# Kernel tuning notes

Measured on AMD Instinct MI355X. Metric: run time of the kernel, lower is better.

The kernel has to match this reference:

```python
import jax, jax.numpy as jnp
import numpy as np

N, E, C_IN, HID, G, L = 100000, 1600000, 64, 32, 128, 3
NEG_SLOPE = 0.01  # F.leaky_relu default


def setup_inputs() -> dict:
    key = jax.random.key(0)
    ks = jax.random.split(key, 10)
    x = jax.random.normal(ks[0], (N, C_IN), dtype=jnp.float32)
    src = jax.random.randint(ks[1], (E,), 0, N, dtype=jnp.int32)
    dst = jax.random.randint(ks[2], (E,), 0, N, dtype=jnp.int32)
    batch = jnp.sort(jax.random.randint(ks[3], (N,), 0, G, dtype=jnp.int32))
    def glorot(k, fan_in, fan_out):
        lim = np.sqrt(6.0 / (fan_in + fan_out)).astype(np.float32)
        return jax.random.uniform(k, (fan_in, fan_out), jnp.float32, -lim, lim)
    W0 = glorot(ks[4], C_IN, HID); b0 = jnp.zeros((HID,), jnp.float32)
    W1 = glorot(ks[5], HID, HID);  b1 = jnp.zeros((HID,), jnp.float32)
    W2 = glorot(ks[6], HID, HID);  b2 = jnp.zeros((HID,), jnp.float32)
    return {"x": x, "W0": W0, "b0": b0, "W1": W1, "b1": b1,
            "W2": W2, "b2": b2, "src": src, "dst": dst, "batch": batch}


def _gcn_conv(x, W, b, src, dst, dinv):
    # PyG GCNConv: h = x W; aggregate with sym-norm (A + I)
    h = x @ W                                   # [N, H]
    coef = (dinv[src] * dinv[dst])[:, None]     # [E, 1]
    msg = h[src] * coef                         # gather + scale
    agg = jax.ops.segment_sum(msg, dst, num_segments=N)
    agg = agg + h * (dinv * dinv)[:, None]      # self-loop term
    return agg + b


def _mean_pool(x, batch, counts):
    s = jax.ops.segment_sum(x, batch, num_segments=G)
    return s / counts[:, None]


def reference(x, W0, b0, W1, b1, W2, b2, src, dst, batch):
    # degree with self loops (edge weight 1), as PyG gcn_norm does
    deg = jax.ops.segment_sum(jnp.ones((E,), x.dtype), dst, num_segments=N) + 1.0
    dinv = jax.lax.rsqrt(deg)
    counts = jnp.maximum(
        jax.ops.segment_sum(jnp.ones((N,), x.dtype), batch, num_segments=G), 1.0)
    params = [(W0, b0), (W1, b1), (W2, b2)]
    feats = []
    h = x
    for W, b in params:
        h = _gcn_conv(h, W, b, src, dst, dinv)
        h = jax.nn.leaky_relu(h, NEG_SLOPE)
        feats.append(_mean_pool(h, batch, counts))
    merge = jnp.mean(jnp.stack(feats, axis=0), axis=0)  # [G, HID]
    return merge
```

## Files before the change

### kernel.cpp

```cpp
#include <hip/hip_runtime.h>
#include <hip/hip_bf16.h>

#define NN 100000
#define NE 1600000
#define CIN 64
#define HIDN 32
#define NG 128
#define SLOPE 0.01f

__global__ __launch_bounds__(256) void k_cnt(const int* __restrict__ batch,
                                             float* __restrict__ cinv) {
  __shared__ int sb[NG + 1];
  int g = threadIdx.x;
  if (g <= NG) {
    int lo = 0, hi = NN;
    while (lo < hi) {
      int mid = (lo + hi) >> 1;
      if (batch[mid] < g) lo = mid + 1; else hi = mid;
    }
    sb[g] = lo;
  }
  __syncthreads();
  if (g < NG) {
    int c = sb[g + 1] - sb[g];
    cinv[g] = 1.0f / (3.0f * fmaxf((float)c, 1.0f));
  }
}


__global__ __launch_bounds__(256) void k_rank(const int* __restrict__ dst,
                                              int* __restrict__ deg,
                                              int* __restrict__ rank) {
  int i = blockIdx.x * 256 + threadIdx.x;
  if (i * 4 >= NE) return;
  int4 d = ((const int4*)dst)[i];
  int4 r;
  r.x = atomicAdd(&deg[d.x], 1);
  r.y = atomicAdd(&deg[d.y], 1);
  r.z = atomicAdd(&deg[d.z], 1);
  r.w = atomicAdd(&deg[d.w], 1);
  ((int4*)rank)[i] = r;
}

__global__ __launch_bounds__(256) void k_norm(const int* __restrict__ deg,
                                              float* __restrict__ dinv) {
  int i = blockIdx.x * 256 + threadIdx.x;
  if (i < NN) dinv[i] = rsqrtf((float)deg[i] + 1.0f);
}


__global__ __launch_bounds__(256) void k_scan1(const int* __restrict__ deg,
                                               int* __restrict__ bsum) {
  __shared__ int s[256];
  int t = threadIdx.x;
  int base = blockIdx.x * 1024 + t * 4;
  int sum = 0;
#pragma unroll
  for (int j = 0; j < 4; ++j) {
    int idx = base + j;
    if (idx < NN) sum += deg[idx];
  }
  s[t] = sum;
  __syncthreads();
  for (int o = 128; o > 0; o >>= 1) {
    if (t < o) s[t] += s[t + o];
    __syncthreads();
  }
  if (t == 0) bsum[blockIdx.x] = s[0];
}

__global__ __launch_bounds__(128) void k_scan2(int* __restrict__ bsum,
                                               int* __restrict__ rowp, int nblk) {
  __shared__ int s[128];
  int t = threadIdx.x;
  if (t < nblk) s[t] = bsum[t];
  __syncthreads();
  if (t == 0) {
    int run = 0;
    for (int i = 0; i < nblk; ++i) {
      int v = s[i];
      s[i] = run;
      run += v;
    }
    rowp[NN] = run;
  }
  __syncthreads();
  if (t < nblk) bsum[t] = s[t];
}

__global__ __launch_bounds__(256) void k_scan3(const int* __restrict__ deg,
                                               const int* __restrict__ bsum,
                                               int* __restrict__ rowp) {
  __shared__ int s[256];
  int t = threadIdx.x;
  int base = blockIdx.x * 1024 + t * 4;
  int d0 = 0, d1 = 0, d2 = 0, d3 = 0;
  if (base < NN) d0 = deg[base];
  if (base + 1 < NN) d1 = deg[base + 1];
  if (base + 2 < NN) d2 = deg[base + 2];
  if (base + 3 < NN) d3 = deg[base + 3];
  int ts = d0 + d1 + d2 + d3;
  s[t] = ts;
  __syncthreads();
  for (int o = 1; o < 256; o <<= 1) {
    int v = (t >= o) ? s[t - o] : 0;
    __syncthreads();
    s[t] += v;
    __syncthreads();
  }
  int run = bsum[blockIdx.x] + s[t] - ts;
  if (base < NN) { rowp[base] = run; run += d0; }
  if (base + 1 < NN) { rowp[base + 1] = run; run += d1; }
  if (base + 2 < NN) { rowp[base + 2] = run; run += d2; }
  if (base + 3 < NN) { rowp[base + 3] = run; run += d3; }
}

__global__ __launch_bounds__(256) void k_scatter(const int* __restrict__ src,
                                                 const int* __restrict__ dst,
                                                 const int* __restrict__ rank,
                                                 const int* __restrict__ rowp,
                                                 int* __restrict__ col) {
  int i = blockIdx.x * 256 + threadIdx.x;
  if (i * 4 >= NE) return;
  int4 d = ((const int4*)dst)[i];
  int4 r = ((const int4*)rank)[i];
  int4 s = ((const int4*)src)[i];
  col[rowp[d.x] + r.x] = s.x;
  col[rowp[d.y] + r.y] = s.y;
  col[rowp[d.z] + r.z] = s.z;
  col[rowp[d.w] + r.w] = s.w;
}


template <int K>
__global__ __launch_bounds__(256) void k_mm(const float* __restrict__ in,
                                            const float* __restrict__ W,
                                            const float* __restrict__ dinv,
                                            __hip_bfloat16* __restrict__ out) {
  __shared__ float sW[K * HIDN];
  int t = threadIdx.x;
  for (int i = t; i < K * HIDN; i += 256) sW[i] = W[i];
  __syncthreads();
  int gid = blockIdx.x * 256 + t;
  int node = gid >> 5;
  int f = gid & 31;
  if (node >= NN) return;
  const float* xr = in + node * K;
  float acc = 0.f;
#pragma unroll
  for (int k = 0; k < K; ++k) acc += xr[k] * sW[k * HIDN + f];
  out[node * HIDN + f] = __float2bfloat16(acc * dinv[node]);
}


template <int WRITE_H>
__global__ __launch_bounds__(256) void k_agg(const __hip_bfloat16* __restrict__ hs,
                                             const int* __restrict__ rowp,
                                             const int* __restrict__ col,
                                             const float* __restrict__ dinv,
                                             const int* __restrict__ batch,
                                             const float* __restrict__ cinv,
                                             const float* __restrict__ bias,
                                             float* __restrict__ hout,
                                             float* __restrict__ pool) {
  const int t = threadIdx.x;
  const int f = t & 31;
  const int sub = t >> 5;
  const float bf = bias[f];
  float pacc = 0.f;
  int gcur = -1;
  const int base = blockIdx.x * 32;
#pragma unroll
  for (int it = 0; it < 4; ++it) {
    const int i = base + it * 8 + sub;
    if (i < NN) {
      float acc = __bfloat162float(hs[i * HIDN + f]);
      const int rs = rowp[i];
      const int re = rowp[i + 1];
      int e = rs;
      for (; e + 4 <= re; e += 4) {
        const int c0 = col[e], c1 = col[e + 1], c2 = col[e + 2], c3 = col[e + 3];
        const float v0 = __bfloat162float(hs[c0 * HIDN + f]);
        const float v1 = __bfloat162float(hs[c1 * HIDN + f]);
        const float v2 = __bfloat162float(hs[c2 * HIDN + f]);
        const float v3 = __bfloat162float(hs[c3 * HIDN + f]);
        acc += (v0 + v1) + (v2 + v3);
      }
      for (; e < re; ++e) acc += __bfloat162float(hs[col[e] * HIDN + f]);
      float v = acc * dinv[i] + bf;
      v = v > 0.f ? v : SLOPE * v;
      if (WRITE_H) hout[i * HIDN + f] = v;
      const int g = batch[i];
      if (g != gcur) {
        if (gcur >= 0) unsafeAtomicAdd(&pool[gcur * HIDN + f], pacc * cinv[gcur]);
        gcur = g;
        pacc = 0.f;
      }
      pacc += v;
    }
  }
  if (gcur >= 0) unsafeAtomicAdd(&pool[gcur * HIDN + f], pacc * cinv[gcur]);
}


extern "C" void kernel_launch(void* const* d_in, const int* in_sizes, int n_in,
                              void* d_out, int out_size, void* d_ws, size_t ws_size,
                              hipStream_t stream) {
  const float* x = (const float*)d_in[0];
  const float* W0 = (const float*)d_in[1];
  const float* b0 = (const float*)d_in[2];
  const float* W1 = (const float*)d_in[3];
  const float* b1 = (const float*)d_in[4];
  const float* W2 = (const float*)d_in[5];
  const float* b2 = (const float*)d_in[6];
  const int* src = (const int*)d_in[7];
  const int* dst = (const int*)d_in[8];
  const int* batch = (const int*)d_in[9];
  float* out = (float*)d_out;

  char* ws = (char*)d_ws;
  auto carve = [&](size_t bytes) -> char* {
    char* p = ws;
    ws += (bytes + 255) & ~(size_t)255;
    return p;
  };
  int* deg = (int*)carve(NN * 4);
  int* rank = (int*)carve((size_t)NE * 4);
  int* rowp = (int*)carve((NN + 1) * 4);
  int* bsum = (int*)carve(128 * 4);
  float* dinv = (float*)carve(NN * 4);
  float* cinv = (float*)carve(NG * 4);
  int* col = (int*)carve((size_t)NE * 4);
  float* hA = (float*)carve((size_t)NN * HIDN * 4);
  __hip_bfloat16* hs = (__hip_bfloat16*)carve((size_t)NN * HIDN * 2);

  hipMemsetAsync(deg, 0, NN * 4, stream);
  hipMemsetAsync(out, 0, NG * HIDN * 4, stream);

  k_cnt<<<1, 256, 0, stream>>>(batch, cinv);

  const int quad_grid = (NE / 4 + 255) / 256;
  k_rank<<<quad_grid, 256, 0, stream>>>(dst, deg, rank);
  k_norm<<<(NN + 255) / 256, 256, 0, stream>>>(deg, dinv);

  int nblk = (NN + 1023) / 1024;
  k_scan1<<<nblk, 256, 0, stream>>>(deg, bsum);
  k_scan2<<<1, 128, 0, stream>>>(bsum, rowp, nblk);
  k_scan3<<<nblk, 256, 0, stream>>>(deg, bsum, rowp);
  k_scatter<<<quad_grid, 256, 0, stream>>>(src, dst, rank, rowp, col);

  const int mm_grid = (NN * HIDN + 255) / 256;
  const int agg_grid = (NN + 31) / 32;

  k_mm<CIN><<<mm_grid, 256, 0, stream>>>(x, W0, dinv, hs);
  k_agg<1><<<agg_grid, 256, 0, stream>>>(hs, rowp, col, dinv, batch, cinv, b0, hA, out);
  k_mm<HIDN><<<mm_grid, 256, 0, stream>>>(hA, W1, dinv, hs);
  k_agg<1><<<agg_grid, 256, 0, stream>>>(hs, rowp, col, dinv, batch, cinv, b1, hA, out);
  k_mm<HIDN><<<mm_grid, 256, 0, stream>>>(hA, W2, dinv, hs);
  k_agg<0><<<agg_grid, 256, 0, stream>>>(hs, rowp, col, dinv, batch, cinv, b2, hA, out);
}
```

Baseline: 468.0 us.

## Fuse setup kernels, split edge kernels into halves, unroll aggregation with nontemporal loads

Folds the graph-count computation into the scan middle kernel and the dinv computation into scan3, removing two launches and one pass over deg. The rank and scatter kernels are each split into two half-size launches on the same stream. The aggregation inner loop gains an 8-wide unrolled path that reads column indices with nontemporal loads, to expose more outstanding gathers and keep index traffic out of cache. The split launches add launch overhead without adding concurrency, since they run in order on one stream.

```diff
diff --git a/kernel.cpp b/kernel.cpp
--- a/kernel.cpp
+++ b/kernel.cpp
@@ -8,31 +8,14 @@
 #define NG 128
 #define SLOPE 0.01f
 
-__global__ __launch_bounds__(256) void k_cnt(const int* __restrict__ batch,
-                                             float* __restrict__ cinv) {
-  __shared__ int sb[NG + 1];
-  int g = threadIdx.x;
-  if (g <= NG) {
-    int lo = 0, hi = NN;
-    while (lo < hi) {
-      int mid = (lo + hi) >> 1;
-      if (batch[mid] < g) lo = mid + 1; else hi = mid;
-    }
-    sb[g] = lo;
-  }
-  __syncthreads();
-  if (g < NG) {
-    int c = sb[g + 1] - sb[g];
-    cinv[g] = 1.0f / (3.0f * fmaxf((float)c, 1.0f));
-  }
-}
-
 
 __global__ __launch_bounds__(256) void k_rank(const int* __restrict__ dst,
                                               int* __restrict__ deg,
-                                              int* __restrict__ rank) {
-  int i = blockIdx.x * 256 + threadIdx.x;
-  if (i * 4 >= NE) return;
+                                              int* __restrict__ rank,
+                                              int qbase, int qcount) {
+  int i0 = blockIdx.x * 256 + threadIdx.x;
+  if (i0 >= qcount) return;
+  int i = qbase + i0;
   int4 d = ((const int4*)dst)[i];
   int4 r;
   r.x = atomicAdd(&deg[d.x], 1);
@@ -42,12 +25,6 @@
   ((int4*)rank)[i] = r;
 }
 
-__global__ __launch_bounds__(256) void k_norm(const int* __restrict__ deg,
-                                              float* __restrict__ dinv) {
-  int i = blockIdx.x * 256 + threadIdx.x;
-  if (i < NN) dinv[i] = rsqrtf((float)deg[i] + 1.0f);
-}
-
 
 __global__ __launch_bounds__(256) void k_scan1(const int* __restrict__ deg,
                                                int* __restrict__ bsum) {
@@ -69,11 +46,22 @@
   if (t == 0) bsum[blockIdx.x] = s[0];
 }
 
-__global__ __launch_bounds__(128) void k_scan2(int* __restrict__ bsum,
-                                               int* __restrict__ rowp, int nblk) {
+__global__ __launch_bounds__(256) void k_mid(int* __restrict__ bsum,
+                                             int* __restrict__ rowp,
+                                             const int* __restrict__ batch,
+                                             float* __restrict__ cinv, int nblk) {
   __shared__ int s[128];
+  __shared__ int sb[NG + 1];
   int t = threadIdx.x;
   if (t < nblk) s[t] = bsum[t];
+  if (t <= NG) {
+    int lo = 0, hi = NN;
+    while (lo < hi) {
+      int mid = (lo + hi) >> 1;
+      if (batch[mid] < t) lo = mid + 1; else hi = mid;
+    }
+    sb[t] = lo;
+  }
   __syncthreads();
   if (t == 0) {
     int run = 0;
@@ -86,11 +74,16 @@
   }
   __syncthreads();
   if (t < nblk) bsum[t] = s[t];
+  if (t < NG) {
+    int c = sb[t + 1] - sb[t];
+    cinv[t] = 1.0f / (3.0f * fmaxf((float)c, 1.0f));
+  }
 }
 
 __global__ __launch_bounds__(256) void k_scan3(const int* __restrict__ deg,
                                                const int* __restrict__ bsum,
-                                               int* __restrict__ rowp) {
+                                               int* __restrict__ rowp,
+                                               float* __restrict__ dinv) {
   __shared__ int s[256];
   int t = threadIdx.x;
   int base = blockIdx.x * 1024 + t * 4;
@@ -109,19 +102,21 @@
     __syncthreads();
   }
   int run = bsum[blockIdx.x] + s[t] - ts;
-  if (base < NN) { rowp[base] = run; run += d0; }
-  if (base + 1 < NN) { rowp[base + 1] = run; run += d1; }
-  if (base + 2 < NN) { rowp[base + 2] = run; run += d2; }
-  if (base + 3 < NN) { rowp[base + 3] = run; run += d3; }
+  if (base < NN) { rowp[base] = run; dinv[base] = rsqrtf((float)d0 + 1.0f); run += d0; }
+  if (base + 1 < NN) { rowp[base + 1] = run; dinv[base + 1] = rsqrtf((float)d1 + 1.0f); run += d1; }
+  if (base + 2 < NN) { rowp[base + 2] = run; dinv[base + 2] = rsqrtf((float)d2 + 1.0f); run += d2; }
+  if (base + 3 < NN) { rowp[base + 3] = run; dinv[base + 3] = rsqrtf((float)d3 + 1.0f); run += d3; }
 }
 
 __global__ __launch_bounds__(256) void k_scatter(const int* __restrict__ src,
                                                  const int* __restrict__ dst,
                                                  const int* __restrict__ rank,
                                                  const int* __restrict__ rowp,
-                                                 int* __restrict__ col) {
-  int i = blockIdx.x * 256 + threadIdx.x;
-  if (i * 4 >= NE) return;
+                                                 int* __restrict__ col,
+                                                 int qbase, int qcount) {
+  int i0 = blockIdx.x * 256 + threadIdx.x;
+  if (i0 >= qcount) return;
+  int i = qbase + i0;
   int4 d = ((const int4*)dst)[i];
   int4 r = ((const int4*)rank)[i];
   int4 s = ((const int4*)src)[i];
@@ -178,8 +173,30 @@
       const int rs = rowp[i];
       const int re = rowp[i + 1];
       int e = rs;
+      for (; e + 8 <= re; e += 8) {
+        const int c0 = __builtin_nontemporal_load(col + e);
+        const int c1 = __builtin_nontemporal_load(col + e + 1);
+        const int c2 = __builtin_nontemporal_load(col + e + 2);
+        const int c3 = __builtin_nontemporal_load(col + e + 3);
+        const int c4 = __builtin_nontemporal_load(col + e + 4);
+        const int c5 = __builtin_nontemporal_load(col + e + 5);
+        const int c6 = __builtin_nontemporal_load(col + e + 6);
+        const int c7 = __builtin_nontemporal_load(col + e + 7);
+        const float v0 = __bfloat162float(hs[c0 * HIDN + f]);
+        const float v1 = __bfloat162float(hs[c1 * HIDN + f]);
+        const float v2 = __bfloat162float(hs[c2 * HIDN + f]);
+        const float v3 = __bfloat162float(hs[c3 * HIDN + f]);
+        const float v4 = __bfloat162float(hs[c4 * HIDN + f]);
+        const float v5 = __bfloat162float(hs[c5 * HIDN + f]);
+        const float v6 = __bfloat162float(hs[c6 * HIDN + f]);
+        const float v7 = __bfloat162float(hs[c7 * HIDN + f]);
+        acc += ((v0 + v1) + (v2 + v3)) + ((v4 + v5) + (v6 + v7));
+      }
       for (; e + 4 <= re; e += 4) {
-        const int c0 = col[e], c1 = col[e + 1], c2 = col[e + 2], c3 = col[e + 3];
+        const int c0 = __builtin_nontemporal_load(col + e);
+        const int c1 = __builtin_nontemporal_load(col + e + 1);
+        const int c2 = __builtin_nontemporal_load(col + e + 2);
+        const int c3 = __builtin_nontemporal_load(col + e + 3);
         const float v0 = __bfloat162float(hs[c0 * HIDN + f]);
         const float v1 = __bfloat162float(hs[c1 * HIDN + f]);
         const float v2 = __bfloat162float(hs[c2 * HIDN + f]);
@@ -237,17 +254,18 @@
   hipMemsetAsync(deg, 0, NN * 4, stream);
   hipMemsetAsync(out, 0, NG * HIDN * 4, stream);
 
-  k_cnt<<<1, 256, 0, stream>>>(batch, cinv);
-
-  const int quad_grid = (NE / 4 + 255) / 256;
-  k_rank<<<quad_grid, 256, 0, stream>>>(dst, deg, rank);
-  k_norm<<<(NN + 255) / 256, 256, 0, stream>>>(deg, dinv);
+  const int QH = NE / 4 / 2;
+  const int half_grid = (QH + 255) / 256;
+  k_rank<<<half_grid, 256, 0, stream>>>(dst, deg, rank, 0, QH);
+  k_rank<<<half_grid, 256, 0, stream>>>(dst, deg, rank, QH, QH);
 
   int nblk = (NN + 1023) / 1024;
   k_scan1<<<nblk, 256, 0, stream>>>(deg, bsum);
-  k_scan2<<<1, 128, 0, stream>>>(bsum, rowp, nblk);
-  k_scan3<<<nblk, 256, 0, stream>>>(deg, bsum, rowp);
-  k_scatter<<<quad_grid, 256, 0, stream>>>(src, dst, rank, rowp, col);
+  k_mid<<<1, 256, 0, stream>>>(bsum, rowp, batch, cinv, nblk);
+  k_scan3<<<nblk, 256, 0, stream>>>(deg, bsum, rowp, dinv);
+
+  k_scatter<<<half_grid, 256, 0, stream>>>(src, dst, rank, rowp, col, 0, QH);
+  k_scatter<<<half_grid, 256, 0, stream>>>(src, dst, rank, rowp, col, QH, QH);
 
   const int mm_grid = (NN * HIDN + 255) / 256;
   const int agg_grid = (NN + 31) / 32;
```

Measured after the change: 473.6 us. About the same (+1.2%).
